# Kernel optimization log

Measured on AMD Instinct MI355X. Metric: run time of the kernel, lower is better.

Reference implementation:

```python
import jax, jax.numpy as jnp
import numpy as np

N_NODES = 50000


def gcn_conv(x, src, dst, W, b, n_nodes):
    """PyG GCNConv: add self-loops, symmetric D^-1/2 (A+I) D^-1/2 normalization,
    linear transform, scatter-add aggregation, bias."""
    loop = jnp.arange(n_nodes, dtype=src.dtype)
    s = jnp.concatenate([src, loop])
    d = jnp.concatenate([dst, loop])
    deg = jax.ops.segment_sum(jnp.ones_like(s, dtype=x.dtype), d, num_segments=n_nodes)
    dinv = jnp.where(deg > 0, jax.lax.rsqrt(deg), 0.0)
    norm = dinv[s] * dinv[d]                      # [E+N]
    h = x @ W                                     # [N, out] dense GEMM first (PyG order)
    msg = h[s] * norm[:, None]                    # gather + scale: [E+N, out]
    out = jax.ops.segment_sum(msg, d, num_segments=n_nodes)  # scatter-add
    return out + b


def setup_inputs() -> dict:
    key = jax.random.key(0)
    k = jax.random.split(key, 4)
    N, E, IN, HID, OUT = N_NODES, 625000, 128, 128, 64
    return {
        "x": jax.random.normal(k[0], (N, IN), jnp.float32),
        "edge_index": jax.random.randint(k[1], (2, E), 0, N, dtype=jnp.int32),
        "W1": jax.random.normal(k[2], (IN, HID), jnp.float32) / np.float32(np.sqrt(IN)),
        "b1": jnp.zeros((HID,), jnp.float32),
        "W2": jax.random.normal(k[3], (HID, OUT), jnp.float32) / np.float32(np.sqrt(HID)),
        "b2": jnp.zeros((OUT,), jnp.float32),
    }


def reference(x, edge_index, W1, b1, W2, b2):
    src, dst = edge_index[0], edge_index[1]
    # n_layers = 2: conv1 + ReLU, then final conv without activation
    h = jax.nn.relu(gcn_conv(x, src, dst, W1, b1, N_NODES))
    return gcn_conv(h, src, dst, W2, b2, N_NODES)
```

## Files before the change

kernel.cpp:

```cpp
#include <hip/hip_runtime.h>
#include <math.h>


#define RPB 32
#define CAP 8192
#define PA_BLK 160

typedef _Float16 h8  __attribute__((ext_vector_type(8)));
typedef _Float16 h2t __attribute__((ext_vector_type(2)));
typedef float    f4v __attribute__((ext_vector_type(4)));

__device__ __forceinline__ unsigned pkh(float a, float b) {
    auto r = __builtin_amdgcn_cvt_pkrtz(a, b);
    return __builtin_bit_cast(unsigned, r);
}
__device__ __forceinline__ void accw(float* g, float c, unsigned w) {
    h2t p = __builtin_bit_cast(h2t, w);
    g[0] += c * (float)p.x;
    g[1] += c * (float)p.y;
}
__device__ __forceinline__ void acc16h(float* ga, float c, uint4 u0, uint4 u1) {
    accw(ga + 0, c, u0.x); accw(ga + 2, c, u0.y);
    accw(ga + 4, c, u0.z); accw(ga + 6, c, u0.w);
    accw(ga + 8, c, u1.x); accw(ga + 10, c, u1.y);
    accw(ga + 12, c, u1.z); accw(ga + 14, c, u1.w);
}
__device__ __forceinline__ void acc8h(float* ga, float c, uint4 u) {
    accw(ga + 0, c, u.x); accw(ga + 2, c, u.y);
    accw(ga + 4, c, u.z); accw(ga + 6, c, u.w);
}

__global__ __launch_bounds__(256) void k_prep(const float* __restrict__ x,
                                              unsigned short* __restrict__ xh, int nElem,
                                              const int* __restrict__ src,
                                              const int* __restrict__ dst, int e,
                                              int* __restrict__ bcur,
                                              int2* __restrict__ ebuf,
                                              int CB, int EPB,
                                              const float* __restrict__ W1,
                                              const float* __restrict__ W2,
                                              unsigned short* __restrict__ Wpk1,
                                              unsigned short* __restrict__ Wpk2) {
    const int blk = (int)blockIdx.x;
    if (blk < CB) {
        int i8 = (blk * 256 + threadIdx.x) * 8;
        if (i8 < nElem) {
            float4 v0 = *(const float4*)&x[i8];
            float4 v1 = *(const float4*)&x[i8 + 4];
            uint4 o;
            o.x = pkh(v0.x, v0.y); o.y = pkh(v0.z, v0.w);
            o.z = pkh(v1.x, v1.y); o.w = pkh(v1.z, v1.w);
            *(uint4*)&xh[i8] = o;
        }
    } else if (blk < CB + PA_BLK) {
        __shared__ int h[256];
        __shared__ int gb[256];
        const int t = threadIdx.x;
        h[t] = 0;
        __syncthreads();
        const int e0 = (blk - CB) * EPB;
        const int e1 = min(e0 + EPB, e);
        for (int i = e0 + t; i < e1; i += 256)
            atomicAdd(&h[((unsigned)dst[i]) >> 8], 1);
        __syncthreads();
        const int c = h[t];
        if (c > 0) gb[t] = atomicAdd(&bcur[t], c);
        h[t] = 0;
        __syncthreads();
        for (int i = e0 + t; i < e1; i += 256) {
            const int d  = dst[i];
            const int bk = ((unsigned)d) >> 8;
            const int p  = atomicAdd(&h[bk], 1) + gb[bk];
            if (p < CAP) ebuf[((size_t)bk << 13) + p] = make_int2(src[i], d);
        }
    } else if (blk < CB + PA_BLK + 8) {
        int idx = (blk - CB - PA_BLK) * 256 + threadIdx.x;
        int l = idx & 63, g = idx >> 6;
        int kt = g >> 3, nt = g & 7;
        const float* Wp = W1 + (size_t)(kt * 32 + ((l >> 4) << 3)) * 128 + nt * 16 + (l & 15);
        uint4 o;
        o.x = pkh(Wp[0],   Wp[128]);
        o.y = pkh(Wp[256], Wp[384]);
        o.z = pkh(Wp[512], Wp[640]);
        o.w = pkh(Wp[768], Wp[896]);
        *(uint4*)&Wpk1[(size_t)idx * 8] = o;
    } else {
        int idx = (blk - CB - PA_BLK - 8) * 256 + threadIdx.x;
        if (idx < 1024) {
            int l = idx & 63, g = idx >> 6;
            int kt = g >> 2, nt = g & 3;
            const float* Wp = W2 + (size_t)(kt * 32 + ((l >> 4) << 3)) * 64 + nt * 16 + (l & 15);
            uint4 o;
            o.x = pkh(Wp[0],   Wp[64]);
            o.y = pkh(Wp[128], Wp[192]);
            o.z = pkh(Wp[256], Wp[320]);
            o.w = pkh(Wp[384], Wp[448]);
            *(uint4*)&Wpk2[(size_t)idx * 8] = o;
        }
    }
}

__global__ __launch_bounds__(256) void k_bucket(const int2* __restrict__ ebuf,
                                                const int* __restrict__ bcur,
                                                int* __restrict__ rowptr,
                                                float* __restrict__ dinv,
                                                int2* __restrict__ erec,
                                                int n, int nbk, int e) {
    __shared__ int sc[256];
    __shared__ int h[256];
    __shared__ int loc[256];
    __shared__ int sBase;
    const int t = threadIdx.x;
    const int b = blockIdx.x;

    const int v = (t < nbk) ? min(bcur[t], CAP) : 0;
    sc[t] = v;
    __syncthreads();
    for (int off = 1; off < 256; off <<= 1) {
        int u = (t >= off) ? sc[t - off] : 0;
        __syncthreads();
        sc[t] += u;
        __syncthreads();
    }
    if (t == b) sBase = sc[t] - v;
    if (b == 0 && t == 0) rowptr[n] = e;
    h[t] = 0;
    __syncthreads();

    const int cb = min(bcur[b], CAP);
    const int2* __restrict__ eb = ebuf + ((size_t)b << 13);
    for (int i = t; i < cb; i += 256) atomicAdd(&h[eb[i].y & 255], 1);
    __syncthreads();
    const int deg = h[t];
    sc[t] = deg;
    __syncthreads();
    for (int off = 1; off < 256; off <<= 1) {
        int u = (t >= off) ? sc[t - off] : 0;
        __syncthreads();
        sc[t] += u;
        __syncthreads();
    }
    loc[t] = sc[t] - deg;
    const int id = (b << 8) + t;
    if (id < n) {
        rowptr[id] = sBase + loc[t];
        dinv[id]   = rsqrtf((float)(deg + 1));
    }
    h[t] = 0;
    __syncthreads();
    int2* __restrict__ outp = erec + sBase;
    for (int i = t; i < cb; i += 256) {
        const int2 r  = eb[i];
        const int  lb = r.y & 255;
        const int  p  = atomicAdd(&h[lb], 1);
        outp[loc[lb] + p] = r;
    }
}

__global__ __launch_bounds__(256) void k_coef(int2* __restrict__ erec,
                                              const float* __restrict__ dinv, int e) {
    int i = blockIdx.x * 256 + threadIdx.x;
    if (i < e) {
        int2 r = erec[i];
        erec[i] = make_int2(r.x, __float_as_int(dinv[r.x] * dinv[r.y]));
    }
}

__global__ __launch_bounds__(256, 4) void fused_l1(const unsigned short* __restrict__ Xh,
                                                   const unsigned short* __restrict__ Wpk1,
                                                   const float* __restrict__ bias1,
                                                   const unsigned short* __restrict__ Wpk2,
                                                   const int* __restrict__ rowptr,
                                                   const int2* __restrict__ erec,
                                                   const float* __restrict__ dinv,
                                                   unsigned short* __restrict__ h2,
                                                   int n) {
    __shared__ __align__(16) char sMb[RPB * 256];

    const int t    = threadIdx.x;
    const int row0 = blockIdx.x * RPB;

    {
        const int r = t >> 3;
        const int b = t & 7;
        const int d = row0 + r;
        float ga[16] = {};
        if (d < n) {
            const float wd = dinv[d];
            const uint4* P = (const uint4*)(Xh + ((size_t)d << 7)) + b * 2;
            acc16h(ga, wd * wd, P[0], P[1]);
            const int beg = rowptr[d], end = rowptr[d + 1];
            int j = beg;
            const int2 Z = make_int2(0, 0);
            int2 r0 = (j     < end) ? erec[j]     : Z;
            int2 r1 = (j + 1 < end) ? erec[j + 1] : Z;
            int2 r2 = (j + 2 < end) ? erec[j + 2] : Z;
            int2 r3 = (j + 3 < end) ? erec[j + 3] : Z;
            while (j < end) {
                const int2 c0 = r0, c1 = r1, c2 = r2, c3 = r3;
                const int jn = j + 4;
                r0 = (jn     < end) ? erec[jn]     : Z;
                r1 = (jn + 1 < end) ? erec[jn + 1] : Z;
                r2 = (jn + 2 < end) ? erec[jn + 2] : Z;
                r3 = (jn + 3 < end) ? erec[jn + 3] : Z;
                const uint4* P0 = (const uint4*)(Xh + ((size_t)c0.x << 7)) + b * 2;
                const uint4* P1 = (const uint4*)(Xh + ((size_t)c1.x << 7)) + b * 2;
                const uint4* P2 = (const uint4*)(Xh + ((size_t)c2.x << 7)) + b * 2;
                const uint4* P3 = (const uint4*)(Xh + ((size_t)c3.x << 7)) + b * 2;
                uint4 a0 = P0[0], a1 = P0[1];
                uint4 b0 = P1[0], b1 = P1[1];
                uint4 d0 = P2[0], d1 = P2[1];
                uint4 e0 = P3[0], e1 = P3[1];
                acc16h(ga, __int_as_float(c0.y), a0, a1);
                acc16h(ga, __int_as_float(c1.y), b0, b1);
                acc16h(ga, __int_as_float(c2.y), d0, d1);
                acc16h(ga, __int_as_float(c3.y), e0, e1);
                j = jn;
            }
        }
        uint4 o0, o1;
        o0.x = pkh(ga[0],  ga[1]);  o0.y = pkh(ga[2],  ga[3]);
        o0.z = pkh(ga[4],  ga[5]);  o0.w = pkh(ga[6],  ga[7]);
        o1.x = pkh(ga[8],  ga[9]);  o1.y = pkh(ga[10], ga[11]);
        o1.z = pkh(ga[12], ga[13]); o1.w = pkh(ga[14], ga[15]);
        const int swz = (r & 7) << 4;
        *(uint4*)(sMb + ((r * 256 + b * 32)      ^ swz)) = o0;
        *(uint4*)(sMb + ((r * 256 + b * 32 + 16) ^ swz)) = o1;
    }
    __syncthreads();

    const int w  = t >> 6;
    const int l  = t & 63;
    const int lr = l & 15;
    const int lk = (l >> 4) << 4;
    const int sz = (lr & 7) << 4;

    f4v acc[2][2] = {};
#pragma unroll
    for (int kt = 0; kt < 4; ++kt) {
        const int kb = kt * 64 + lk;
        h8 a0 = *(const h8*)(sMb + ((lr * 256 + kb)        ^ sz));
        h8 a1 = *(const h8*)(sMb + (((lr + 16) * 256 + kb) ^ sz));
        const h8* Bp = (const h8*)Wpk1 + (kt * 8 + w * 2) * 64 + l;
        h8 b0 = Bp[0];
        h8 b1 = Bp[64];
        acc[0][0] = __builtin_amdgcn_mfma_f32_16x16x32_f16(a0, b0, acc[0][0], 0, 0, 0);
        acc[0][1] = __builtin_amdgcn_mfma_f32_16x16x32_f16(a0, b1, acc[0][1], 0, 0, 0);
        acc[1][0] = __builtin_amdgcn_mfma_f32_16x16x32_f16(a1, b0, acc[1][0], 0, 0, 0);
        acc[1][1] = __builtin_amdgcn_mfma_f32_16x16x32_f16(a1, b1, acc[1][1], 0, 0, 0);
    }
    __syncthreads();

    {
        const float bb0 = bias1[w * 32 + lr];
        const float bb1 = bias1[w * 32 + 16 + lr];
        const int c0 = (w * 32 + lr) * 2;
        const int c1 = (w * 32 + 16 + lr) * 2;
#pragma unroll
        for (int mt = 0; mt < 2; ++mt)
#pragma unroll
            for (int v = 0; v < 4; ++v) {
                const int row = mt * 16 + ((l >> 4) << 2) + v;
                const int rs  = (row & 7) << 4;
                float o0 = fmaxf(acc[mt][0][v] + bb0, 0.f);
                float o1 = fmaxf(acc[mt][1][v] + bb1, 0.f);
                *(_Float16*)(sMb + ((row * 256 + c0) ^ rs)) = (_Float16)o0;
                *(_Float16*)(sMb + ((row * 256 + c1) ^ rs)) = (_Float16)o1;
            }
    }
    __syncthreads();

    f4v acc2[2] = {};
#pragma unroll
    for (int kt = 0; kt < 4; ++kt) {
        const int kb = kt * 64 + lk;
        h8 a0 = *(const h8*)(sMb + ((lr * 256 + kb)        ^ sz));
        h8 a1 = *(const h8*)(sMb + (((lr + 16) * 256 + kb) ^ sz));
        h8 b  = *((const h8*)Wpk2 + (kt * 4 + w) * 64 + l);
        acc2[0] = __builtin_amdgcn_mfma_f32_16x16x32_f16(a0, b, acc2[0], 0, 0, 0);
        acc2[1] = __builtin_amdgcn_mfma_f32_16x16x32_f16(a1, b, acc2[1], 0, 0, 0);
    }
#pragma unroll
    for (int mt = 0; mt < 2; ++mt)
#pragma unroll
        for (int v = 0; v < 4; ++v) {
            const int row = row0 + mt * 16 + ((l >> 4) << 2) + v;
            if (row < n) {
                _Float16 hv = (_Float16)acc2[mt][v];
                h2[(size_t)row * 64 + w * 16 + lr] = __builtin_bit_cast(unsigned short, hv);
            }
        }
}

__global__ __launch_bounds__(256, 6) void k_out(const unsigned short* __restrict__ h2,
                                                const float* __restrict__ b2,
                                                const int* __restrict__ rowptr,
                                                const int2* __restrict__ erec,
                                                const float* __restrict__ dinv,
                                                float* __restrict__ out, int n) {
    const int t = threadIdx.x;
    const int r = t >> 3;
    const int b = t & 7;
    const int d = blockIdx.x * RPB + r;
    if (d >= n) return;

    float ga[8] = {};
    {
        const float wd = dinv[d];
        uint4 u = *((const uint4*)(h2 + ((size_t)d << 6)) + b);
        acc8h(ga, wd * wd, u);
    }
    const int beg = rowptr[d], end = rowptr[d + 1];
    int j = beg;
    const int2 Z = make_int2(0, 0);
    int2 r0 = (j     < end) ? erec[j]     : Z;
    int2 r1 = (j + 1 < end) ? erec[j + 1] : Z;
    int2 r2 = (j + 2 < end) ? erec[j + 2] : Z;
    int2 r3 = (j + 3 < end) ? erec[j + 3] : Z;
    while (j < end) {
        const int2 c0 = r0, c1 = r1, c2 = r2, c3 = r3;
        const int jn = j + 4;
        r0 = (jn     < end) ? erec[jn]     : Z;
        r1 = (jn + 1 < end) ? erec[jn + 1] : Z;
        r2 = (jn + 2 < end) ? erec[jn + 2] : Z;
        r3 = (jn + 3 < end) ? erec[jn + 3] : Z;
        uint4 a  = *((const uint4*)(h2 + ((size_t)c0.x << 6)) + b);
        uint4 u1 = *((const uint4*)(h2 + ((size_t)c1.x << 6)) + b);
        uint4 u2 = *((const uint4*)(h2 + ((size_t)c2.x << 6)) + b);
        uint4 u3 = *((const uint4*)(h2 + ((size_t)c3.x << 6)) + b);
        acc8h(ga, __int_as_float(c0.y), a);
        acc8h(ga, __int_as_float(c1.y), u1);
        acc8h(ga, __int_as_float(c2.y), u2);
        acc8h(ga, __int_as_float(c3.y), u3);
        j = jn;
    }
    const float4 bv0 = *(const float4*)&b2[b * 8];
    const float4 bv1 = *(const float4*)&b2[b * 8 + 4];
    float* O = out + (size_t)d * 64 + b * 8;
    *(float4*)O       = make_float4(ga[0] + bv0.x, ga[1] + bv0.y, ga[2] + bv0.z, ga[3] + bv0.w);
    *(float4*)(O + 4) = make_float4(ga[4] + bv1.x, ga[5] + bv1.y, ga[6] + bv1.z, ga[7] + bv1.w);
}


extern "C" void kernel_launch(void* const* d_in, const int* in_sizes, int n_in,
                              void* d_out, int out_size, void* d_ws, size_t ws_size,
                              hipStream_t stream) {
    const float* x  = (const float*)d_in[0];
    const int*   ei = (const int*)d_in[1];
    const float* W1 = (const float*)d_in[2];
    const float* b1 = (const float*)d_in[3];
    const float* W2 = (const float*)d_in[4];
    const float* b2 = (const float*)d_in[5];
    float* out = (float*)d_out;

    const int N = in_sizes[0] / 128;
    const int E = in_sizes[1] / 2;
    const int* src = ei;
    const int* dst = ei + E;
    const int NBK = (N + 255) >> 8;
    if (NBK > 256) return;

    size_t off = 0;
    char* base = (char*)d_ws;
    auto carve = [&](size_t bytes) -> void* {
        void* p = base + off;
        off += (bytes + 255) & ~(size_t)255;
        return p;
    };
    int*   bcur   = (int*)carve(256 * 4);
    int*   rowptr = (int*)carve((size_t)(N + 1) * 4);
    float* dinv   = (float*)carve((size_t)N * 4);
    int2*  erec   = (int2*)carve((size_t)E * 8);
    int2*  ebuf   = (int2*)carve((size_t)256 * CAP * 8);
    unsigned short* xh   = (unsigned short*)carve((size_t)N * 128 * 2);
    unsigned short* h2   = (unsigned short*)carve((size_t)N * 64 * 2);
    unsigned short* Wpk1 = (unsigned short*)carve(128 * 128 * 2);
    unsigned short* Wpk2 = (unsigned short*)carve(128 * 64 * 2);

    if (off > ws_size) return;

    const int nElem = N * 128;
    const int CB  = (nElem / 8 + 255) / 256;
    const int EPB = (E + PA_BLK - 1) / PA_BLK;
    hipMemsetAsync(bcur, 0, 256 * 4, stream);
    k_prep<<<CB + PA_BLK + 12, 256, 0, stream>>>(x, xh, nElem, src, dst, E,
                                                 bcur, ebuf, CB, EPB,
                                                 W1, W2, Wpk1, Wpk2);
    k_bucket<<<NBK, 256, 0, stream>>>(ebuf, bcur, rowptr, dinv, erec, N, NBK, E);
    k_coef<<<(E + 255) / 256, 256, 0, stream>>>(erec, dinv, E);

    const int nblk = (N + RPB - 1) / RPB;
    fused_l1<<<nblk, 256, 0, stream>>>(xh, Wpk1, b1, Wpk2, rowptr, erec, dinv, h2, N);
    k_out<<<nblk, 256, 0, stream>>>(h2, b2, rowptr, erec, dinv, out, N);
}
```

Baseline: 160.7 us.

## Factor symmetric normalization into pre-scaled features and pack edges to 32-bit

Replaces per-edge norm coefficients with source-side dinv scaling folded into the fp16 feature copies (x and h2) and destination-side dinv applied once per row, removing the k_coef kernel. Edge records shrink from int2 (src, coef) to a single 32-bit src index, with the dst low byte packed into the top bits during bucketing, which halves edge-stream traffic in bucketing and both aggregation passes. The x conversion moves out of k_prep into a new k_scale kernel that runs after dinv exists, and also writes a zero padding row used for out-of-range tail loads. Occupancy hints and PA_BLK are raised. The packing limits source indices to 24 bits, and fp16 rounding now applies to pre-scaled values.

Result: slower. 190.0 us (+18.3%).

```diff
diff --git a/kernel.cpp b/kernel.cpp
--- a/kernel.cpp
+++ b/kernel.cpp
@@ -4,7 +4,7 @@
 
 #define RPB 32
 #define CAP 8192
-#define PA_BLK 160
+#define PA_BLK 256
 
 typedef _Float16 h8  __attribute__((ext_vector_type(8)));
 typedef _Float16 h2t __attribute__((ext_vector_type(2)));
@@ -30,35 +30,22 @@
     accw(ga + 4, c, u.z); accw(ga + 6, c, u.w);
 }
 
-__global__ __launch_bounds__(256) void k_prep(const float* __restrict__ x,
-                                              unsigned short* __restrict__ xh, int nElem,
-                                              const int* __restrict__ src,
+__global__ __launch_bounds__(256) void k_prep(const int* __restrict__ src,
                                               const int* __restrict__ dst, int e,
                                               int* __restrict__ bcur,
-                                              int2* __restrict__ ebuf,
-                                              int CB, int EPB,
+                                              unsigned* __restrict__ ebuf, int EPB,
                                               const float* __restrict__ W1,
                                               const float* __restrict__ W2,
                                               unsigned short* __restrict__ Wpk1,
                                               unsigned short* __restrict__ Wpk2) {
     const int blk = (int)blockIdx.x;
-    if (blk < CB) {
-        int i8 = (blk * 256 + threadIdx.x) * 8;
-        if (i8 < nElem) {
-            float4 v0 = *(const float4*)&x[i8];
-            float4 v1 = *(const float4*)&x[i8 + 4];
-            uint4 o;
-            o.x = pkh(v0.x, v0.y); o.y = pkh(v0.z, v0.w);
-            o.z = pkh(v1.x, v1.y); o.w = pkh(v1.z, v1.w);
-            *(uint4*)&xh[i8] = o;
-        }
-    } else if (blk < CB + PA_BLK) {
+    if (blk < PA_BLK) {
         __shared__ int h[256];
         __shared__ int gb[256];
         const int t = threadIdx.x;
         h[t] = 0;
         __syncthreads();
-        const int e0 = (blk - CB) * EPB;
+        const int e0 = blk * EPB;
         const int e1 = min(e0 + EPB, e);
         for (int i = e0 + t; i < e1; i += 256)
             atomicAdd(&h[((unsigned)dst[i]) >> 8], 1);
@@ -68,13 +55,13 @@
         h[t] = 0;
         __syncthreads();
         for (int i = e0 + t; i < e1; i += 256) {
-            const int d  = dst[i];
-            const int bk = ((unsigned)d) >> 8;
+            const unsigned d  = (unsigned)dst[i];
+            const int bk = d >> 8;
             const int p  = atomicAdd(&h[bk], 1) + gb[bk];
-            if (p < CAP) ebuf[((size_t)bk << 13) + p] = make_int2(src[i], d);
+            if (p < CAP) ebuf[((size_t)bk << 13) + p] = ((d & 255u) << 24) | (unsigned)src[i];
         }
-    } else if (blk < CB + PA_BLK + 8) {
-        int idx = (blk - CB - PA_BLK) * 256 + threadIdx.x;
+    } else if (blk < PA_BLK + 8) {
+        int idx = (blk - PA_BLK) * 256 + threadIdx.x;
         int l = idx & 63, g = idx >> 6;
         int kt = g >> 3, nt = g & 7;
         const float* Wp = W1 + (size_t)(kt * 32 + ((l >> 4) << 3)) * 128 + nt * 16 + (l & 15);
@@ -85,7 +72,7 @@
         o.w = pkh(Wp[768], Wp[896]);
         *(uint4*)&Wpk1[(size_t)idx * 8] = o;
     } else {
-        int idx = (blk - CB - PA_BLK - 8) * 256 + threadIdx.x;
+        int idx = (blk - PA_BLK - 8) * 256 + threadIdx.x;
         if (idx < 1024) {
             int l = idx & 63, g = idx >> 6;
             int kt = g >> 2, nt = g & 3;
@@ -100,11 +87,11 @@
     }
 }
 
-__global__ __launch_bounds__(256) void k_bucket(const int2* __restrict__ ebuf,
+__global__ __launch_bounds__(256) void k_bucket(const unsigned* __restrict__ ebuf,
                                                 const int* __restrict__ bcur,
                                                 int* __restrict__ rowptr,
                                                 float* __restrict__ dinv,
-                                                int2* __restrict__ erec,
+                                                unsigned* __restrict__ erec,
                                                 int n, int nbk, int e) {
     __shared__ int sc[256];
     __shared__ int h[256];
@@ -128,8 +115,8 @@
     __syncthreads();
 
     const int cb = min(bcur[b], CAP);
-    const int2* __restrict__ eb = ebuf + ((size_t)b << 13);
-    for (int i = t; i < cb; i += 256) atomicAdd(&h[eb[i].y & 255], 1);
+    const unsigned* __restrict__ eb = ebuf + ((size_t)b << 13);
+    for (int i = t; i < cb; i += 256) atomicAdd(&h[eb[i] >> 24], 1);
     __syncthreads();
     const int deg = h[t];
     sc[t] = deg;
@@ -148,32 +135,46 @@
     }
     h[t] = 0;
     __syncthreads();
-    int2* __restrict__ outp = erec + sBase;
+    unsigned* __restrict__ outp = erec + sBase;
     for (int i = t; i < cb; i += 256) {
-        const int2 r  = eb[i];
-        const int  lb = r.y & 255;
-        const int  p  = atomicAdd(&h[lb], 1);
-        outp[loc[lb] + p] = r;
-    }
-}
-
-__global__ __launch_bounds__(256) void k_coef(int2* __restrict__ erec,
-                                              const float* __restrict__ dinv, int e) {
-    int i = blockIdx.x * 256 + threadIdx.x;
-    if (i < e) {
-        int2 r = erec[i];
-        erec[i] = make_int2(r.x, __float_as_int(dinv[r.x] * dinv[r.y]));
-    }
-}
-
-__global__ __launch_bounds__(256, 4) void fused_l1(const unsigned short* __restrict__ Xh,
+        const unsigned r  = eb[i];
+        const int      lb = r >> 24;
+        const int      p  = atomicAdd(&h[lb], 1);
+        outp[loc[lb] + p] = r & 0xFFFFFFu;
+    }
+}
+
+__global__ __launch_bounds__(256) void k_scale(const float* __restrict__ x,
+                                               const float* __restrict__ dinv,
+                                               unsigned short* __restrict__ xs,
+                                               unsigned short* __restrict__ h2s,
+                                               int n) {
+    const int gid = blockIdx.x * 256 + threadIdx.x;
+    const int i8  = gid * 8;
+    const int row = i8 >> 7;
+    if (row < n) {
+        const float wd = dinv[row];
+        float4 v0 = *(const float4*)&x[i8];
+        float4 v1 = *(const float4*)&x[i8 + 4];
+        uint4 o;
+        o.x = pkh(v0.x * wd, v0.y * wd); o.y = pkh(v0.z * wd, v0.w * wd);
+        o.z = pkh(v1.x * wd, v1.y * wd); o.w = pkh(v1.z * wd, v1.w * wd);
+        *(uint4*)&xs[i8] = o;
+    } else if (row == n) {
+        *(uint4*)&xs[i8] = make_uint4(0, 0, 0, 0);
+        const int k = gid - n * 16;
+        if (k < 8) *(uint4*)&h2s[(size_t)n * 64 + k * 8] = make_uint4(0, 0, 0, 0);
+    }
+}
+
+__global__ __launch_bounds__(256, 6) void fused_l1(const unsigned short* __restrict__ Xs,
                                                    const unsigned short* __restrict__ Wpk1,
                                                    const float* __restrict__ bias1,
                                                    const unsigned short* __restrict__ Wpk2,
                                                    const int* __restrict__ rowptr,
-                                                   const int2* __restrict__ erec,
+                                                   const unsigned* __restrict__ erec,
                                                    const float* __restrict__ dinv,
-                                                   unsigned short* __restrict__ h2,
+                                                   unsigned short* __restrict__ h2s,
                                                    int n) {
     __shared__ __align__(16) char sMb[RPB * 256];
 
@@ -187,34 +188,34 @@
         float ga[16] = {};
         if (d < n) {
             const float wd = dinv[d];
-            const uint4* P = (const uint4*)(Xh + ((size_t)d << 7)) + b * 2;
-            acc16h(ga, wd * wd, P[0], P[1]);
+            const uint4* P = (const uint4*)(Xs + ((size_t)d << 7)) + b * 2;
+            acc16h(ga, wd, P[0], P[1]);
             const int beg = rowptr[d], end = rowptr[d + 1];
             int j = beg;
-            const int2 Z = make_int2(0, 0);
-            int2 r0 = (j     < end) ? erec[j]     : Z;
-            int2 r1 = (j + 1 < end) ? erec[j + 1] : Z;
-            int2 r2 = (j + 2 < end) ? erec[j + 2] : Z;
-            int2 r3 = (j + 3 < end) ? erec[j + 3] : Z;
+            const unsigned Z = (unsigned)n;
+            unsigned s0 = (j     < end) ? erec[j]     : Z;
+            unsigned s1 = (j + 1 < end) ? erec[j + 1] : Z;
+            unsigned s2 = (j + 2 < end) ? erec[j + 2] : Z;
+            unsigned s3 = (j + 3 < end) ? erec[j + 3] : Z;
             while (j < end) {
-                const int2 c0 = r0, c1 = r1, c2 = r2, c3 = r3;
+                const unsigned c0 = s0, c1 = s1, c2 = s2, c3 = s3;
                 const int jn = j + 4;
-                r0 = (jn     < end) ? erec[jn]     : Z;
-                r1 = (jn + 1 < end) ? erec[jn + 1] : Z;
-                r2 = (jn + 2 < end) ? erec[jn + 2] : Z;
-                r3 = (jn + 3 < end) ? erec[jn + 3] : Z;
-                const uint4* P0 = (const uint4*)(Xh + ((size_t)c0.x << 7)) + b * 2;
-                const uint4* P1 = (const uint4*)(Xh + ((size_t)c1.x << 7)) + b * 2;
-                const uint4* P2 = (const uint4*)(Xh + ((size_t)c2.x << 7)) + b * 2;
-                const uint4* P3 = (const uint4*)(Xh + ((size_t)c3.x << 7)) + b * 2;
+                s0 = (jn     < end) ? erec[jn]     : Z;
+                s1 = (jn + 1 < end) ? erec[jn + 1] : Z;
+                s2 = (jn + 2 < end) ? erec[jn + 2] : Z;
+                s3 = (jn + 3 < end) ? erec[jn + 3] : Z;
+                const uint4* P0 = (const uint4*)(Xs + ((size_t)c0 << 7)) + b * 2;
+                const uint4* P1 = (const uint4*)(Xs + ((size_t)c1 << 7)) + b * 2;
+                const uint4* P2 = (const uint4*)(Xs + ((size_t)c2 << 7)) + b * 2;
+                const uint4* P3 = (const uint4*)(Xs + ((size_t)c3 << 7)) + b * 2;
                 uint4 a0 = P0[0], a1 = P0[1];
                 uint4 b0 = P1[0], b1 = P1[1];
                 uint4 d0 = P2[0], d1 = P2[1];
                 uint4 e0 = P3[0], e1 = P3[1];
-                acc16h(ga, __int_as_float(c0.y), a0, a1);
-                acc16h(ga, __int_as_float(c1.y), b0, b1);
-                acc16h(ga, __int_as_float(c2.y), d0, d1);
-                acc16h(ga, __int_as_float(c3.y), e0, e1);
+                acc16h(ga, wd, a0, a1);
+                acc16h(ga, wd, b0, b1);
+                acc16h(ga, wd, d0, d1);
+                acc16h(ga, wd, e0, e1);
                 j = jn;
             }
         }
@@ -286,16 +287,16 @@
         for (int v = 0; v < 4; ++v) {
             const int row = row0 + mt * 16 + ((l >> 4) << 2) + v;
             if (row < n) {
-                _Float16 hv = (_Float16)acc2[mt][v];
-                h2[(size_t)row * 64 + w * 16 + lr] = __builtin_bit_cast(unsigned short, hv);
+                _Float16 hv = (_Float16)(acc2[mt][v] * dinv[row]);
+                h2s[(size_t)row * 64 + w * 16 + lr] = __builtin_bit_cast(unsigned short, hv);
             }
         }
 }
 
-__global__ __launch_bounds__(256, 6) void k_out(const unsigned short* __restrict__ h2,
+__global__ __launch_bounds__(256, 8) void k_out(const unsigned short* __restrict__ h2s,
                                                 const float* __restrict__ b2,
                                                 const int* __restrict__ rowptr,
-                                                const int2* __restrict__ erec,
+                                                const unsigned* __restrict__ erec,
                                                 const float* __restrict__ dinv,
                                                 float* __restrict__ out, int n) {
     const int t = threadIdx.x;
@@ -304,34 +305,34 @@
     const int d = blockIdx.x * RPB + r;
     if (d >= n) return;
 
+    const float wd = dinv[d];
     float ga[8] = {};
     {
-        const float wd = dinv[d];
-        uint4 u = *((const uint4*)(h2 + ((size_t)d << 6)) + b);
-        acc8h(ga, wd * wd, u);
+        uint4 u = *((const uint4*)(h2s + ((size_t)d << 6)) + b);
+        acc8h(ga, wd, u);
     }
     const int beg = rowptr[d], end = rowptr[d + 1];
     int j = beg;
-    const int2 Z = make_int2(0, 0);
-    int2 r0 = (j     < end) ? erec[j]     : Z;
-    int2 r1 = (j + 1 < end) ? erec[j + 1] : Z;
-    int2 r2 = (j + 2 < end) ? erec[j + 2] : Z;
-    int2 r3 = (j + 3 < end) ? erec[j + 3] : Z;
+    const unsigned Z = (unsigned)n;
+    unsigned s0 = (j     < end) ? erec[j]     : Z;
+    unsigned s1 = (j + 1 < end) ? erec[j + 1] : Z;
+    unsigned s2 = (j + 2 < end) ? erec[j + 2] : Z;
+    unsigned s3 = (j + 3 < end) ? erec[j + 3] : Z;
     while (j < end) {
-        const int2 c0 = r0, c1 = r1, c2 = r2, c3 = r3;
+        const unsigned c0 = s0, c1 = s1, c2 = s2, c3 = s3;
         const int jn = j + 4;
-        r0 = (jn     < end) ? erec[jn]     : Z;
-        r1 = (jn + 1 < end) ? erec[jn + 1] : Z;
-        r2 = (jn + 2 < end) ? erec[jn + 2] : Z;
-        r3 = (jn + 3 < end) ? erec[jn + 3] : Z;
-        uint4 a  = *((const uint4*)(h2 + ((size_t)c0.x << 6)) + b);
-        uint4 u1 = *((const uint4*)(h2 + ((size_t)c1.x << 6)) + b);
-        uint4 u2 = *((const uint4*)(h2 + ((size_t)c2.x << 6)) + b);
-        uint4 u3 = *((const uint4*)(h2 + ((size_t)c3.x << 6)) + b);
-        acc8h(ga, __int_as_float(c0.y), a);
-        acc8h(ga, __int_as_float(c1.y), u1);
-        acc8h(ga, __int_as_float(c2.y), u2);
-        acc8h(ga, __int_as_float(c3.y), u3);
+        s0 = (jn     < end) ? erec[jn]     : Z;
+        s1 = (jn + 1 < end) ? erec[jn + 1] : Z;
+        s2 = (jn + 2 < end) ? erec[jn + 2] : Z;
+        s3 = (jn + 3 < end) ? erec[jn + 3] : Z;
+        uint4 u0 = *((const uint4*)(h2s + ((size_t)c0 << 6)) + b);
+        uint4 u1 = *((const uint4*)(h2s + ((size_t)c1 << 6)) + b);
+        uint4 u2 = *((const uint4*)(h2s + ((size_t)c2 << 6)) + b);
+        uint4 u3 = *((const uint4*)(h2s + ((size_t)c3 << 6)) + b);
+        acc8h(ga, wd, u0);
+        acc8h(ga, wd, u1);
+        acc8h(ga, wd, u2);
+        acc8h(ga, wd, u3);
         j = jn;
     }
     const float4 bv0 = *(const float4*)&b2[b * 8];
@@ -367,29 +368,26 @@
         off += (bytes + 255) & ~(size_t)255;
         return p;
     };
-    int*   bcur   = (int*)carve(256 * 4);
-    int*   rowptr = (int*)carve((size_t)(N + 1) * 4);
-    float* dinv   = (float*)carve((size_t)N * 4);
-    int2*  erec   = (int2*)carve((size_t)E * 8);
-    int2*  ebuf   = (int2*)carve((size_t)256 * CAP * 8);
-    unsigned short* xh   = (unsigned short*)carve((size_t)N * 128 * 2);
-    unsigned short* h2   = (unsigned short*)carve((size_t)N * 64 * 2);
+    int*      bcur   = (int*)carve(256 * 4);
+    int*      rowptr = (int*)carve((size_t)(N + 1) * 4);
+    float*    dinv   = (float*)carve((size_t)N * 4);
+    unsigned* erec   = (unsigned*)carve((size_t)E * 4);
+    unsigned* ebuf   = (unsigned*)carve((size_t)256 * CAP * 4);
+    unsigned short* xs   = (unsigned short*)carve((size_t)(N + 1) * 128 * 2);
+    unsigned short* h2s  = (unsigned short*)carve((size_t)(N + 1) * 64 * 2);
     unsigned short* Wpk1 = (unsigned short*)carve(128 * 128 * 2);
     unsigned short* Wpk2 = (unsigned short*)carve(128 * 64 * 2);
 
     if (off > ws_size) return;
 
-    const int nElem = N * 128;
-    const int CB  = (nElem / 8 + 255) / 256;
     const int EPB = (E + PA_BLK - 1) / PA_BLK;
     hipMemsetAsync(bcur, 0, 256 * 4, stream);
-    k_prep<<<CB + PA_BLK + 12, 256, 0, stream>>>(x, xh, nElem, src, dst, E,
-                                                 bcur, ebuf, CB, EPB,
-                                                 W1, W2, Wpk1, Wpk2);
+    k_prep<<<PA_BLK + 12, 256, 0, stream>>>(src, dst, E, bcur, ebuf, EPB,
+                                            W1, W2, Wpk1, Wpk2);
     k_bucket<<<NBK, 256, 0, stream>>>(ebuf, bcur, rowptr, dinv, erec, N, NBK, E);
-    k_coef<<<(E + 255) / 256, 256, 0, stream>>>(erec, dinv, E);
+    k_scale<<<((N + 1) * 16 + 255) / 256, 256, 0, stream>>>(x, dinv, xs, h2s, N);
 
     const int nblk = (N + RPB - 1) / RPB;
-    fused_l1<<<nblk, 256, 0, stream>>>(xh, Wpk1, b1, Wpk2, rowptr, erec, dinv, h2, N);
-    k_out<<<nblk, 256, 0, stream>>>(h2, b2, rowptr, erec, dinv, out, N);
-}
+    fused_l1<<<nblk, 256, 0, stream>>>(xs, Wpk1, b1, Wpk2, rowptr, erec, dinv, h2s, N);
+    k_out<<<nblk, 256, 0, stream>>>(h2s, b2, rowptr, erec, dinv, out, N);
+}
```
